# Optimization experiments

Measured on AMD Instinct MI355X. Metric: run time of the kernel, lower is better.

## Reference

```python
import jax, jax.numpy as jnp
import numpy as np

# Static geometry constants (match input_specs / init_kwargs)
B, NP, C_IN = 16, 4096, 64          # clouds, points per cloud, feature dim
RATIO, RAD = 0.25, 0.2
M = int(RATIO * NP)
HID, OUT = 64, 128


def setup_inputs() -> dict:
    key = jax.random.key(0)
    ks = jax.random.split(key, 8)
    point = jax.random.uniform(ks[0], (B * NP, 3), dtype=jnp.float32)
    xyz = jax.random.normal(ks[1], (B * NP, C_IN), dtype=jnp.float32)
    batch = jnp.arange(B * NP, dtype=jnp.int32) // NP  # contiguous equal-size clouds
    s = 0.05
    W1 = jax.random.normal(ks[2], (C_IN + 3, HID), dtype=jnp.float32) * s
    b1 = jnp.zeros((HID,), jnp.float32)
    W2 = jax.random.normal(ks[3], (HID, HID), dtype=jnp.float32) * s
    b2 = jnp.zeros((HID,), jnp.float32)
    W3 = jax.random.normal(ks[4], (HID, OUT), dtype=jnp.float32) * s
    b3 = jnp.zeros((OUT,), jnp.float32)
    return {"xyz": xyz, "point": point, "batch": batch, "num_samples": 64,
            "W1": W1, "b1": b1, "W2": W2, "b2": b2, "W3": W3, "b3": b3}


def _fps(p):
    """Farthest point sampling on one cloud p:[NP,3] -> [M] local indices (start at 0)."""
    d0 = jnp.sum((p - p[0]) ** 2, axis=-1)
    def step(d, _):
        nxt = jnp.argmax(d).astype(jnp.int32)
        d = jnp.minimum(d, jnp.sum((p - p[nxt]) ** 2, axis=-1))
        return d, nxt
    _, rest = jax.lax.scan(step, d0, None, length=M - 1)
    return jnp.concatenate([jnp.zeros((1,), jnp.int32), rest])


def reference(xyz, point, batch, num_samples, W1, b1, W2, b2, W3, b3):
    K = int(num_samples)
    pos = point.reshape(B, NP, 3)
    feat = xyz.reshape(B, NP, C_IN)

    # fps(point, batch, ratio)
    idx = jax.vmap(_fps)(pos)                                      # [B,M]
    centers = jnp.take_along_axis(pos, idx[..., None], axis=1)      # [B,M,3]

    # radius(point, point[idx], rad, max_num_neighbors=K): take K nearest in-ball
    d2 = jnp.sum((centers[:, :, None, :] - pos[:, None, :, :]) ** 2, axis=-1)  # [B,M,NP]
    valid = d2 < RAD * RAD
    sel = jnp.where(valid, d2, jnp.inf)
    _, nidx = jax.lax.top_k(-jax.lax.stop_gradient(sel), K)         # [B,M,K]
    mask = jnp.take_along_axis(valid, nidx, axis=2)                 # [B,M,K]

    # PointConv: msg = local_nn(cat([x_j, pos_j - pos_i])), aggr = max
    bi = jnp.arange(B)[:, None, None]
    pos_j = pos[bi, nidx]                                           # [B,M,K,3]
    feat_j = feat[bi, nidx]                                         # [B,M,K,C]
    msg = jnp.concatenate([feat_j, pos_j - centers[:, :, None, :]], axis=-1)
    h = jax.nn.relu(msg @ W1 + b1)
    h = jax.nn.relu(h @ W2 + b2)
    h = jax.nn.relu(h @ W3 + b3)                                    # [B,M,K,OUT]
    h = jnp.where(mask[..., None], h, -jnp.inf)
    out = jnp.max(h, axis=2).reshape(B * M, OUT)

    idx_g = (idx + jnp.arange(B, dtype=jnp.int32)[:, None] * NP).reshape(-1)
    return out, centers.reshape(B * M, 3), batch[idx_g]
```

## Files before the change

kernel.cpp:

```cpp
#include <hip/hip_runtime.h>
#include <cstdint>

#define NB 16
#define NP 4096
#define MC 1024
#define KNN 64
#define CIN 64
#define HID 64
#define OUTD 128

typedef __attribute__((ext_vector_type(8))) short bf16x8;
typedef __attribute__((ext_vector_type(4))) float f32x4;
typedef __attribute__((ext_vector_type(2))) float f32x2;
typedef unsigned long long ull;
typedef unsigned short ushort_t;

#define F32_INF __int_as_float(0x7f800000)

__device__ __forceinline__ float dist2e(float ax, float ay, float az,
                                        float bx, float by, float bz) {
  float dx = __fsub_rn(ax, bx);
  float dy = __fsub_rn(ay, by);
  float dz = __fsub_rn(az, bz);
  return __fadd_rn(__fadd_rn(__fmul_rn(dx, dx), __fmul_rn(dy, dy)), __fmul_rn(dz, dz));
}

__device__ __forceinline__ ushort_t f2bf(float f) {
  unsigned u = __float_as_uint(f);
  unsigned r = (u + 0x7FFFu + ((u >> 16) & 1u)) >> 16;
  return (ushort_t)r;
}

template <int CTRL>
__device__ __forceinline__ ull kshift(ull k) {
  int lo = (int)(unsigned)(k & 0xffffffffULL);
  int hi = (int)(unsigned)(k >> 32);
  lo = __builtin_amdgcn_update_dpp(lo, lo, CTRL, 0xf, 0xf, false);
  hi = __builtin_amdgcn_update_dpp(hi, hi, CTRL, 0xf, 0xf, false);
  return ((ull)(unsigned)hi << 32) | (ull)(unsigned)lo;
}
template <int CTRL>
__device__ __forceinline__ ull kred(ull k) {
  ull o = kshift<CTRL>(k);
  return (o > k) ? o : k;
}

__device__ __forceinline__ void wfrag_entry(const float* __restrict__ W,
                                            ushort_t* __restrict__ out,
                                            int e, int KS, int K, int N) {
  int lane = e & 63, t2 = e >> 6;
  int ks = t2 % KS, nt = t2 / KS;
  int n = nt * 16 + (lane & 15);
  int kb = ks * 32 + ((lane >> 4) & 3) * 8;
#pragma unroll
  for (int j = 0; j < 8; ++j) {
    int k = kb + j;
    float v = (k < K) ? W[(size_t)k * N + n] : 0.f;
    out[(size_t)e * 8 + j] = f2bf(v);
  }
}

__global__ __launch_bounds__(256) void fps_prep_kernel(
    const float* __restrict__ point, const float* __restrict__ xyz,
    const float* __restrict__ W1, const float* __restrict__ W2, const float* __restrict__ W3,
    float* __restrict__ ctr, float* __restrict__ cent_out, float* __restrict__ batch_out,
    ushort_t* __restrict__ xyzbf, ushort_t* __restrict__ w1f,
    ushort_t* __restrict__ w2f, ushort_t* __restrict__ w3f) {
#pragma clang fp contract(off)
  const int blk = blockIdx.x;
  const int t = threadIdx.x;
  if (blk >= NB) {
    const int pb = blk - NB;
    if (pb < 4096) {
      size_t i = ((size_t)pb * 256 + t) * 4;
      float4 v = *(const float4*)(xyz + i);
      unsigned lo = (unsigned)f2bf(v.x) | ((unsigned)f2bf(v.y) << 16);
      unsigned hi = (unsigned)f2bf(v.z) | ((unsigned)f2bf(v.w) << 16);
      uint2 o; o.x = lo; o.y = hi;
      *(uint2*)(xyzbf + i) = o;
    } else {
      for (int e = t; e < 4 * 3 * 64; e += 256) wfrag_entry(W1, w1f, e, 3, CIN + 3, HID);
      for (int e = t; e < 4 * 2 * 64; e += 256) wfrag_entry(W2, w2f, e, 2, HID, HID);
      for (int e = t; e < 8 * 2 * 64; e += 256) wfrag_entry(W3, w3f, e, 2, HID, OUTD);
    }
    return;
  }
  const int b = blk;
  const int lane = t & 63, wid = t >> 6;
  __shared__ float4 pts[NP];
  __shared__ ull kbuf[2][4];
  __shared__ int whist[MC];
  const float* p = point + (size_t)b * NP * 3;
  for (int i = t; i < NP; i += 256) {
    float4 v; v.x = p[3 * i]; v.y = p[3 * i + 1]; v.z = p[3 * i + 2]; v.w = 0.f;
    pts[i] = v;
  }
  if (t == 0) whist[0] = 0;
  __syncthreads();
  f32x2 qx2[8], qy2[8], qz2[8], d2v[8];
#pragma unroll
  for (int k = 0; k < 8; ++k) {
    float4 v0 = pts[t * 16 + 2 * k];
    float4 v1 = pts[t * 16 + 2 * k + 1];
    qx2[k].x = v0.x; qx2[k].y = v1.x;
    qy2[k].x = v0.y; qy2[k].y = v1.y;
    qz2[k].x = v0.z; qz2[k].y = v1.z;
    d2v[k].x = F32_INF; d2v[k].y = F32_INF;
  }
  int w = 0;
  for (int it = 1; it < MC; ++it) {
    float4 wp = pts[w];
    f32x2 wxx; wxx.x = wp.x; wxx.y = wp.x;
    f32x2 wyy; wyy.x = wp.y; wyy.y = wp.y;
    f32x2 wzz; wzz.x = wp.z; wzz.y = wp.z;
    float bd = -1.0f; int br = 0;
#pragma unroll
    for (int k = 0; k < 8; ++k) {
      f32x2 dx = qx2[k] - wxx;
      f32x2 dy = qy2[k] - wyy;
      f32x2 dz = qz2[k] - wzz;
      f32x2 nd = (dx * dx + dy * dy) + dz * dz;
      f32x2 dv;
      dv.x = fminf(d2v[k].x, nd.x);
      dv.y = fminf(d2v[k].y, nd.y);
      d2v[k] = dv;
      bool p1 = dv.y > dv.x;
      float pd = p1 ? dv.y : dv.x;
      int pr = 2 * k + (p1 ? 1 : 0);
      if (pd > bd) { bd = pd; br = pr; }
    }
    unsigned gi = (unsigned)(t * 16 + br);
    ull key = ((ull)__float_as_uint(bd) << 32) | (ull)(unsigned)~gi;
    key = kred<0x111>(key);
    key = kred<0x112>(key);
    key = kred<0x114>(key);
    key = kred<0x118>(key);
    key = kred<0x142>(key);
    key = kred<0x143>(key);
    const int par = it & 1;
    if (lane == 63) kbuf[par][wid] = key;
    __syncthreads();
    ull k0 = kbuf[par][0], k1 = kbuf[par][1], k2 = kbuf[par][2], k3 = kbuf[par][3];
    ull ka = (k0 > k1) ? k0 : k1;
    ull kb = (k2 > k3) ? k2 : k3;
    ull km = (ka > kb) ? ka : kb;
    w = (int)~(unsigned)(km & 0xffffffffULL);
    if (t == 0) whist[it] = w;
  }
  __syncthreads();
  for (int s = t; s < MC; s += 256) {
    int wi = whist[s];
    float4 wp = pts[wi];
    size_t o = (size_t)b * MC + s;
    ctr[3*o] = wp.x; ctr[3*o+1] = wp.y; ctr[3*o+2] = wp.z;
    cent_out[3*o] = wp.x; cent_out[3*o+1] = wp.y; cent_out[3*o+2] = wp.z;
    batch_out[o] = (float)b;
  }
}

__global__ void neigh_kernel(const float* __restrict__ point,
                             const float* __restrict__ ctr,
                             int* __restrict__ nidx, int* __restrict__ ncnt) {
  const int c = blockIdx.x;
  const int b = c >> 10;
  const int lane = threadIdx.x;
  __shared__ float ld[512];
  __shared__ int li[512];
  const float R2 = (float)(0.2 * 0.2);
  const float cx = ctr[3*c], cy = ctr[3*c+1], cz = ctr[3*c+2];
  const float* p = point + (size_t)b * NP * 3;
  int cnt = 0;
  for (int s = 0; s < NP / 64; ++s) {
    int j = s * 64 + lane;
    float d2 = dist2e(cx, cy, cz, p[3*j], p[3*j+1], p[3*j+2]);
    bool v = d2 < R2;
    ull m = __ballot(v);
    if (v) {
      int pos = cnt + __popcll(m & ((1ull << lane) - 1ull));
      if (pos < 512) { ld[pos] = d2; li[pos] = j; }
    }
    cnt += __popcll(m);
  }
  if (cnt > 512) cnt = 512;
  __syncthreads();
  if (cnt <= KNN) {
    nidx[(size_t)c * KNN + lane] = (lane < cnt) ? li[lane] : 0;
  } else {
    unsigned ob[8]; int oi[8];
#pragma unroll
    for (int r = 0; r < 8; ++r) {
      int s2 = lane + r * 64;
      if (s2 < cnt) { ob[r] = __float_as_uint(ld[s2]); oi[r] = li[s2]; }
      else { ob[r] = 0xFFFFFFFFu; oi[r] = 0; }
    }
    unsigned L = 0u, H = 0x3D23D70Au;
    while (L < H) {
      unsigned mid = (L + H) >> 1;
      int cle = 0;
#pragma unroll
      for (int r = 0; r < 8; ++r) cle += (int)__popcll(__ballot(ob[r] <= mid));
      if (cle >= KNN) H = mid; else L = mid + 1;
    }
    const unsigned tau = H;
    int c_lt = 0;
#pragma unroll
    for (int r = 0; r < 8; ++r) c_lt += (int)__popcll(__ballot(ob[r] < tau));
    const int need = KNN - c_lt;
    const ull below = (1ull << lane) - 1ull;
    int outpos = 0, eqc = 0;
#pragma unroll
    for (int r = 0; r < 8; ++r) {
      ull meq = __ballot(ob[r] == tau);
      int eqrank = eqc + (int)__popcll(meq & below);
      bool sel = (ob[r] < tau) || ((ob[r] == tau) && (eqrank < need));
      ull msel = __ballot(sel);
      if (sel) {
        int posn = outpos + (int)__popcll(msel & below);
        nidx[(size_t)c * KNN + posn] = oi[r];
      }
      outpos += (int)__popcll(msel);
      eqc += (int)__popcll(meq);
    }
  }
  if (lane == 0) ncnt[c] = (cnt < KNN) ? cnt : KNN;
}

#define HSTRIDE 72
__global__ __launch_bounds__(256) void mlp_kernel(
    const ushort_t* __restrict__ xyzbf, const float* __restrict__ point,
    const float* __restrict__ ctr, const int* __restrict__ nidx,
    const int* __restrict__ ncnt,
    const ushort_t* __restrict__ w1f, const ushort_t* __restrict__ w2f,
    const ushort_t* __restrict__ w3f,
    const float* __restrict__ b1, const float* __restrict__ b2,
    const float* __restrict__ b3,
    float* __restrict__ out) {
  const int wv = threadIdx.x >> 6, lane = threadIdx.x & 63;
  const int quad = lane >> 4, col16 = lane & 15;
  const int c = blockIdx.x * 4 + wv;
  const int bcl = c >> 10;
  const size_t bbase = (size_t)bcl * NP;
  __shared__ ushort_t hbuf_all[4 * 64 * HSTRIDE];
  ushort_t* hb = hbuf_all + wv * 64 * HSTRIDE;

  const int jg = nidx[(size_t)c * KNN + lane];
  const int nv = ncnt[c];
  const float cx = ctr[3*c], cy = ctr[3*c+1], cz = ctr[3*c+2];
  const float* pp = point + (bbase + jg) * 3;
  const float dx = pp[0] - cx, dy = pp[1] - cy, dz = pp[2] - cz;

  bf16x8 a1[4][2];
  bf16x8 a2[4];
#pragma unroll
  for (int mt = 0; mt < 4; ++mt) {
    int srcl = mt * 16 + col16;
    int jmt = __shfl(jg, srcl);
    const ushort_t* rp = xyzbf + (bbase + (size_t)jmt) * CIN + quad * 8;
    a1[mt][0] = *(const bf16x8*)(rp);
    a1[mt][1] = *(const bf16x8*)(rp + 32);
    float ddx = __shfl(dx, srcl), ddy = __shfl(dy, srcl), ddz = __shfl(dz, srcl);
    bf16x8 t2 = {0, 0, 0, 0, 0, 0, 0, 0};
    if (quad == 0) {
      t2[0] = (short)f2bf(ddx); t2[1] = (short)f2bf(ddy); t2[2] = (short)f2bf(ddz);
    }
    a2[mt] = t2;
  }

  bf16x8 bw1[4][3];
#pragma unroll
  for (int nt = 0; nt < 4; ++nt)
#pragma unroll
    for (int ks = 0; ks < 3; ++ks)
      bw1[nt][ks] = *(const bf16x8*)(w1f + ((size_t)(nt * 3 + ks) * 64 + lane) * 8);
  f32x4 acc1[4][4];
#pragma unroll
  for (int nt = 0; nt < 4; ++nt) {
    float bv = b1[nt * 16 + col16];
#pragma unroll
    for (int mt = 0; mt < 4; ++mt) { f32x4 v = {bv, bv, bv, bv}; acc1[mt][nt] = v; }
  }
#pragma unroll
  for (int mt = 0; mt < 4; ++mt)
#pragma unroll
    for (int nt = 0; nt < 4; ++nt) {
      acc1[mt][nt] = __builtin_amdgcn_mfma_f32_16x16x32_bf16(a1[mt][0], bw1[nt][0], acc1[mt][nt], 0, 0, 0);
      acc1[mt][nt] = __builtin_amdgcn_mfma_f32_16x16x32_bf16(a1[mt][1], bw1[nt][1], acc1[mt][nt], 0, 0, 0);
      acc1[mt][nt] = __builtin_amdgcn_mfma_f32_16x16x32_bf16(a2[mt],    bw1[nt][2], acc1[mt][nt], 0, 0, 0);
    }
#pragma unroll
  for (int mt = 0; mt < 4; ++mt)
#pragma unroll
    for (int nt = 0; nt < 4; ++nt)
#pragma unroll
      for (int reg = 0; reg < 4; ++reg) {
        int row = quad * 4 + reg + mt * 16;
        hb[row * HSTRIDE + col16 + nt * 16] = f2bf(fmaxf(acc1[mt][nt][reg], 0.f));
      }

  bf16x8 a21[4][2];
#pragma unroll
  for (int mt = 0; mt < 4; ++mt)
#pragma unroll
    for (int ks = 0; ks < 2; ++ks)
      a21[mt][ks] = *(const bf16x8*)(hb + (col16 + mt * 16) * HSTRIDE + ks * 32 + quad * 8);
  bf16x8 bw2[4][2];
#pragma unroll
  for (int nt = 0; nt < 4; ++nt)
#pragma unroll
    for (int ks = 0; ks < 2; ++ks)
      bw2[nt][ks] = *(const bf16x8*)(w2f + ((size_t)(nt * 2 + ks) * 64 + lane) * 8);
  f32x4 acc2[4][4];
#pragma unroll
  for (int nt = 0; nt < 4; ++nt) {
    float bv = b2[nt * 16 + col16];
#pragma unroll
    for (int mt = 0; mt < 4; ++mt) { f32x4 v = {bv, bv, bv, bv}; acc2[mt][nt] = v; }
  }
#pragma unroll
  for (int mt = 0; mt < 4; ++mt)
#pragma unroll
    for (int nt = 0; nt < 4; ++nt) {
      acc2[mt][nt] = __builtin_amdgcn_mfma_f32_16x16x32_bf16(a21[mt][0], bw2[nt][0], acc2[mt][nt], 0, 0, 0);
      acc2[mt][nt] = __builtin_amdgcn_mfma_f32_16x16x32_bf16(a21[mt][1], bw2[nt][1], acc2[mt][nt], 0, 0, 0);
    }
#pragma unroll
  for (int mt = 0; mt < 4; ++mt)
#pragma unroll
    for (int nt = 0; nt < 4; ++nt)
#pragma unroll
      for (int reg = 0; reg < 4; ++reg) {
        int row = quad * 4 + reg + mt * 16;
        hb[row * HSTRIDE + col16 + nt * 16] = f2bf(fmaxf(acc2[mt][nt][reg], 0.f));
      }

  bf16x8 a3[4][2];
#pragma unroll
  for (int mt = 0; mt < 4; ++mt)
#pragma unroll
    for (int ks = 0; ks < 2; ++ks)
      a3[mt][ks] = *(const bf16x8*)(hb + (col16 + mt * 16) * HSTRIDE + ks * 32 + quad * 8);
#pragma unroll
  for (int pass = 0; pass < 2; ++pass) {
    bf16x8 bw3[4][2];
#pragma unroll
    for (int nt = 0; nt < 4; ++nt)
#pragma unroll
      for (int ks = 0; ks < 2; ++ks)
        bw3[nt][ks] = *(const bf16x8*)(w3f + ((size_t)((pass * 4 + nt) * 2 + ks) * 64 + lane) * 8);
    f32x4 acc3[4][4];
#pragma unroll
    for (int nt = 0; nt < 4; ++nt) {
      float bv = b3[pass * 64 + nt * 16 + col16];
#pragma unroll
      for (int mt = 0; mt < 4; ++mt) { f32x4 v = {bv, bv, bv, bv}; acc3[mt][nt] = v; }
    }
#pragma unroll
    for (int mt = 0; mt < 4; ++mt)
#pragma unroll
      for (int nt = 0; nt < 4; ++nt) {
        acc3[mt][nt] = __builtin_amdgcn_mfma_f32_16x16x32_bf16(a3[mt][0], bw3[nt][0], acc3[mt][nt], 0, 0, 0);
        acc3[mt][nt] = __builtin_amdgcn_mfma_f32_16x16x32_bf16(a3[mt][1], bw3[nt][1], acc3[mt][nt], 0, 0, 0);
      }
#pragma unroll
    for (int nt = 0; nt < 4; ++nt) {
      float m = -1.0e30f;
#pragma unroll
      for (int mt = 0; mt < 4; ++mt)
#pragma unroll
        for (int reg = 0; reg < 4; ++reg) {
          int row = quad * 4 + reg + mt * 16;
          float v = fmaxf(acc3[mt][nt][reg], 0.f);
          m = fmaxf(m, (row < nv) ? v : -1.0e30f);
        }
      m = fmaxf(m, __shfl_xor(m, 16));
      m = fmaxf(m, __shfl_xor(m, 32));
      if (quad == 0)
        out[(size_t)c * OUTD + pass * 64 + nt * 16 + col16] = m;
    }
  }
}

extern "C" void kernel_launch(void* const* d_in, const int* in_sizes, int n_in,
                              void* d_out, int out_size, void* d_ws, size_t ws_size,
                              hipStream_t stream) {
  const float* xyz   = (const float*)d_in[0];
  const float* point = (const float*)d_in[1];
  const float* W1 = (const float*)d_in[4];
  const float* b1 = (const float*)d_in[5];
  const float* W2 = (const float*)d_in[6];
  const float* b2 = (const float*)d_in[7];
  const float* W3 = (const float*)d_in[8];
  const float* b3 = (const float*)d_in[9];

  float* out       = (float*)d_out;
  float* cent_out  = out + (size_t)NB * MC * OUTD;
  float* batch_out = cent_out + (size_t)NB * MC * 3;

  char* ws = (char*)d_ws;
  float* ctr       = (float*)(ws);
  int*   nidx      = (int*)(ws + 196608);
  int*   ncnt      = (int*)(ws + 196608 + 4194304);
  ushort_t* xyzbf  = (ushort_t*)(ws + 4456448);
  ushort_t* w1f    = (ushort_t*)(ws + 4456448 + 8388608);
  ushort_t* w2f    = (ushort_t*)(ws + 12845056 + 12288);
  ushort_t* w3f    = (ushort_t*)(ws + 12857344 + 8192);

  fps_prep_kernel<<<NB + 4096 + 1, 256, 0, stream>>>(
      point, xyz, W1, W2, W3, ctr, cent_out, batch_out, xyzbf, w1f, w2f, w3f);
  neigh_kernel<<<NB * MC, 64, 0, stream>>>(point, ctr, nidx, ncnt);
  mlp_kernel<<<NB * MC / 4, 256, 0, stream>>>(xyzbf, point, ctr, nidx, ncnt,
                                              w1f, w2f, w3f, b1, b2, b3, out);
}
```

Measured before the change: 850.1 us.

## Fuse FPS, neighbor search and MLP into persistent kernel with streamed center flags

Replaces the three-kernel pipeline with one persistent kernel. Sixteen blocks run farthest point sampling and publish each chosen index to global memory as soon as it is picked. The remaining 240 blocks poll those flags, then do the ball query and the MLP per center in the same wave, keeping weight fragments in LDS. This overlaps the long serial FPS with the neighbor/MLP work and drops the nidx/ctr and bf16 xyz workspace round-trips, at the cost of spin-waiting, on-the-fly bf16 conversion of features, and a reliance on FPS blocks being co-resident with the consumer blocks (256 blocks total) so the polling cannot deadlock.

```diff
diff --git a/kernel.cpp b/kernel.cpp
--- a/kernel.cpp
+++ b/kernel.cpp
@@ -16,6 +16,7 @@
 typedef unsigned short ushort_t;
 
 #define F32_INF __int_as_float(0x7f800000)
+#define WSENT 0xFFFFFFFFu
 
 __device__ __forceinline__ float dist2e(float ax, float ay, float az,
                                         float bx, float by, float bz) {
@@ -60,322 +61,341 @@
   }
 }
 
-__global__ __launch_bounds__(256) void fps_prep_kernel(
+__global__ void init_widx(unsigned* __restrict__ widx) {
+  int i = blockIdx.x * 256 + threadIdx.x;
+  if (i < NB * MC) widx[i] = WSENT;
+}
+
+__global__ __launch_bounds__(256) void mega_kernel(
     const float* __restrict__ point, const float* __restrict__ xyz,
     const float* __restrict__ W1, const float* __restrict__ W2, const float* __restrict__ W3,
-    float* __restrict__ ctr, float* __restrict__ cent_out, float* __restrict__ batch_out,
-    ushort_t* __restrict__ xyzbf, ushort_t* __restrict__ w1f,
-    ushort_t* __restrict__ w2f, ushort_t* __restrict__ w3f) {
+    const float* __restrict__ b1, const float* __restrict__ b2, const float* __restrict__ b3,
+    unsigned* __restrict__ widx,
+    float* __restrict__ out, float* __restrict__ cent_out, float* __restrict__ batch_out) {
 #pragma clang fp contract(off)
+  __shared__ char __attribute__((aligned(16))) smem[74752];
   const int blk = blockIdx.x;
   const int t = threadIdx.x;
-  if (blk >= NB) {
-    const int pb = blk - NB;
-    if (pb < 4096) {
-      size_t i = ((size_t)pb * 256 + t) * 4;
-      float4 v = *(const float4*)(xyz + i);
-      unsigned lo = (unsigned)f2bf(v.x) | ((unsigned)f2bf(v.y) << 16);
-      unsigned hi = (unsigned)f2bf(v.z) | ((unsigned)f2bf(v.w) << 16);
-      uint2 o; o.x = lo; o.y = hi;
-      *(uint2*)(xyzbf + i) = o;
-    } else {
-      for (int e = t; e < 4 * 3 * 64; e += 256) wfrag_entry(W1, w1f, e, 3, CIN + 3, HID);
-      for (int e = t; e < 4 * 2 * 64; e += 256) wfrag_entry(W2, w2f, e, 2, HID, HID);
-      for (int e = t; e < 8 * 2 * 64; e += 256) wfrag_entry(W3, w3f, e, 2, HID, OUTD);
+
+  if (blk < NB) {
+    const int b = blk;
+    const int lane = t & 63, wid = t >> 6;
+    float4* pts = (float4*)smem;
+    ull* kbuf = (ull*)(smem + 65536);
+    int* whist = (int*)(smem + 65600);
+    const float* p = point + (size_t)b * NP * 3;
+    for (int i = t; i < NP; i += 256) {
+      float4 v; v.x = p[3 * i]; v.y = p[3 * i + 1]; v.z = p[3 * i + 2]; v.w = 0.f;
+      pts[i] = v;
+    }
+    if (t == 0) {
+      whist[0] = 0;
+      __hip_atomic_store(widx + (size_t)b * MC, 0u, __ATOMIC_RELAXED, __HIP_MEMORY_SCOPE_AGENT);
+    }
+    __syncthreads();
+    f32x2 qx2[8], qy2[8], qz2[8], d2v[8];
+#pragma unroll
+    for (int k = 0; k < 8; ++k) {
+      float4 v0 = pts[t * 16 + 2 * k];
+      float4 v1 = pts[t * 16 + 2 * k + 1];
+      qx2[k].x = v0.x; qx2[k].y = v1.x;
+      qy2[k].x = v0.y; qy2[k].y = v1.y;
+      qz2[k].x = v0.z; qz2[k].y = v1.z;
+      d2v[k].x = F32_INF; d2v[k].y = F32_INF;
+    }
+    int w = 0;
+    for (int it = 1; it < MC; ++it) {
+      float4 wp = pts[w];
+      f32x2 wxx; wxx.x = wp.x; wxx.y = wp.x;
+      f32x2 wyy; wyy.x = wp.y; wyy.y = wp.y;
+      f32x2 wzz; wzz.x = wp.z; wzz.y = wp.z;
+      float bd = -1.0f; int br = 0;
+#pragma unroll
+      for (int k = 0; k < 8; ++k) {
+        f32x2 dx = qx2[k] - wxx;
+        f32x2 dy = qy2[k] - wyy;
+        f32x2 dz = qz2[k] - wzz;
+        f32x2 nd = (dx * dx + dy * dy) + dz * dz;
+        f32x2 dv;
+        dv.x = fminf(d2v[k].x, nd.x);
+        dv.y = fminf(d2v[k].y, nd.y);
+        d2v[k] = dv;
+        bool p1 = dv.y > dv.x;
+        float pd = p1 ? dv.y : dv.x;
+        int pr = 2 * k + (p1 ? 1 : 0);
+        if (pd > bd) { bd = pd; br = pr; }
+      }
+      unsigned gi = (unsigned)(t * 16 + br);
+      ull key = ((ull)__float_as_uint(bd) << 32) | (ull)(unsigned)~gi;
+      key = kred<0x111>(key);
+      key = kred<0x112>(key);
+      key = kred<0x114>(key);
+      key = kred<0x118>(key);
+      key = kred<0x142>(key);
+      key = kred<0x143>(key);
+      const int par = it & 1;
+      if (lane == 63) kbuf[par * 4 + wid] = key;
+      __syncthreads();
+      ull k0 = kbuf[par * 4 + 0], k1 = kbuf[par * 4 + 1];
+      ull k2 = kbuf[par * 4 + 2], k3 = kbuf[par * 4 + 3];
+      ull ka = (k0 > k1) ? k0 : k1;
+      ull kb = (k2 > k3) ? k2 : k3;
+      ull km = (ka > kb) ? ka : kb;
+      w = (int)~(unsigned)(km & 0xffffffffULL);
+      if (t == 0) {
+        whist[it] = w;
+        __hip_atomic_store(widx + (size_t)b * MC + it, (unsigned)w,
+                           __ATOMIC_RELAXED, __HIP_MEMORY_SCOPE_AGENT);
+      }
+    }
+    __syncthreads();
+    for (int s = t; s < MC; s += 256) {
+      int wi = whist[s];
+      float4 wp = pts[wi];
+      size_t o = (size_t)b * MC + s;
+      cent_out[3*o] = wp.x; cent_out[3*o+1] = wp.y; cent_out[3*o+2] = wp.z;
+      batch_out[o] = (float)b;
     }
     return;
   }
-  const int b = blk;
-  const int lane = t & 63, wid = t >> 6;
-  __shared__ float4 pts[NP];
-  __shared__ ull kbuf[2][4];
-  __shared__ int whist[MC];
-  const float* p = point + (size_t)b * NP * 3;
-  for (int i = t; i < NP; i += 256) {
-    float4 v; v.x = p[3 * i]; v.y = p[3 * i + 1]; v.z = p[3 * i + 2]; v.w = 0.f;
-    pts[i] = v;
-  }
-  if (t == 0) whist[0] = 0;
+
+  const int wv = t >> 6, lane = t & 63;
+  const int quad = lane >> 4, col16 = lane & 15;
+  ushort_t* w1L = (ushort_t*)smem;
+  ushort_t* w2L = (ushort_t*)(smem + 12288);
+  ushort_t* w3L = (ushort_t*)(smem + 20480);
+  for (int e = t; e < 4 * 3 * 64; e += 256) wfrag_entry(W1, w1L, e, 3, CIN + 3, HID);
+  for (int e = t; e < 4 * 2 * 64; e += 256) wfrag_entry(W2, w2L, e, 2, HID, HID);
+  for (int e = t; e < 8 * 2 * 64; e += 256) wfrag_entry(W3, w3L, e, 2, HID, OUTD);
   __syncthreads();
-  f32x2 qx2[8], qy2[8], qz2[8], d2v[8];
-#pragma unroll
-  for (int k = 0; k < 8; ++k) {
-    float4 v0 = pts[t * 16 + 2 * k];
-    float4 v1 = pts[t * 16 + 2 * k + 1];
-    qx2[k].x = v0.x; qx2[k].y = v1.x;
-    qy2[k].x = v0.y; qy2[k].y = v1.y;
-    qz2[k].x = v0.z; qz2[k].y = v1.z;
-    d2v[k].x = F32_INF; d2v[k].y = F32_INF;
-  }
-  int w = 0;
-  for (int it = 1; it < MC; ++it) {
-    float4 wp = pts[w];
-    f32x2 wxx; wxx.x = wp.x; wxx.y = wp.x;
-    f32x2 wyy; wyy.x = wp.y; wyy.y = wp.y;
-    f32x2 wzz; wzz.x = wp.z; wzz.y = wp.z;
-    float bd = -1.0f; int br = 0;
-#pragma unroll
-    for (int k = 0; k < 8; ++k) {
-      f32x2 dx = qx2[k] - wxx;
-      f32x2 dy = qy2[k] - wyy;
-      f32x2 dz = qz2[k] - wzz;
-      f32x2 nd = (dx * dx + dy * dy) + dz * dz;
-      f32x2 dv;
-      dv.x = fminf(d2v[k].x, nd.x);
-      dv.y = fminf(d2v[k].y, nd.y);
-      d2v[k] = dv;
-      bool p1 = dv.y > dv.x;
-      float pd = p1 ? dv.y : dv.x;
-      int pr = 2 * k + (p1 ? 1 : 0);
-      if (pd > bd) { bd = pd; br = pr; }
-    }
-    unsigned gi = (unsigned)(t * 16 + br);
-    ull key = ((ull)__float_as_uint(bd) << 32) | (ull)(unsigned)~gi;
-    key = kred<0x111>(key);
-    key = kred<0x112>(key);
-    key = kred<0x114>(key);
-    key = kred<0x118>(key);
-    key = kred<0x142>(key);
-    key = kred<0x143>(key);
-    const int par = it & 1;
-    if (lane == 63) kbuf[par][wid] = key;
-    __syncthreads();
-    ull k0 = kbuf[par][0], k1 = kbuf[par][1], k2 = kbuf[par][2], k3 = kbuf[par][3];
-    ull ka = (k0 > k1) ? k0 : k1;
-    ull kb = (k2 > k3) ? k2 : k3;
-    ull km = (ka > kb) ? ka : kb;
-    w = (int)~(unsigned)(km & 0xffffffffULL);
-    if (t == 0) whist[it] = w;
-  }
-  __syncthreads();
-  for (int s = t; s < MC; s += 256) {
-    int wi = whist[s];
-    float4 wp = pts[wi];
-    size_t o = (size_t)b * MC + s;
-    ctr[3*o] = wp.x; ctr[3*o+1] = wp.y; ctr[3*o+2] = wp.z;
-    cent_out[3*o] = wp.x; cent_out[3*o+1] = wp.y; cent_out[3*o+2] = wp.z;
-    batch_out[o] = (float)b;
-  }
-}
-
-__global__ void neigh_kernel(const float* __restrict__ point,
-                             const float* __restrict__ ctr,
-                             int* __restrict__ nidx, int* __restrict__ ncnt) {
-  const int c = blockIdx.x;
-  const int b = c >> 10;
-  const int lane = threadIdx.x;
-  __shared__ float ld[512];
-  __shared__ int li[512];
+
+  char* base = smem + 36864 + wv * 9472;
+  float* ld = (float*)base;
+  int* li = (int*)(base + 2048);
+  ushort_t* hb = (ushort_t*)base;
+  int* nsel = (int*)(base + 9216);
   const float R2 = (float)(0.2 * 0.2);
-  const float cx = ctr[3*c], cy = ctr[3*c+1], cz = ctr[3*c+2];
-  const float* p = point + (size_t)b * NP * 3;
-  int cnt = 0;
-  for (int s = 0; s < NP / 64; ++s) {
-    int j = s * 64 + lane;
-    float d2 = dist2e(cx, cy, cz, p[3*j], p[3*j+1], p[3*j+2]);
-    bool v = d2 < R2;
-    ull m = __ballot(v);
-    if (v) {
-      int pos = cnt + __popcll(m & ((1ull << lane) - 1ull));
-      if (pos < 512) { ld[pos] = d2; li[pos] = j; }
-    }
-    cnt += __popcll(m);
-  }
-  if (cnt > 512) cnt = 512;
-  __syncthreads();
-  if (cnt <= KNN) {
-    nidx[(size_t)c * KNN + lane] = (lane < cnt) ? li[lane] : 0;
-  } else {
-    unsigned ob[8]; int oi[8];
-#pragma unroll
-    for (int r = 0; r < 8; ++r) {
-      int s2 = lane + r * 64;
-      if (s2 < cnt) { ob[r] = __float_as_uint(ld[s2]); oi[r] = li[s2]; }
-      else { ob[r] = 0xFFFFFFFFu; oi[r] = 0; }
-    }
-    unsigned L = 0u, H = 0x3D23D70Au;
-    while (L < H) {
-      unsigned mid = (L + H) >> 1;
-      int cle = 0;
-#pragma unroll
-      for (int r = 0; r < 8; ++r) cle += (int)__popcll(__ballot(ob[r] <= mid));
-      if (cle >= KNN) H = mid; else L = mid + 1;
-    }
-    const unsigned tau = H;
-    int c_lt = 0;
-#pragma unroll
-    for (int r = 0; r < 8; ++r) c_lt += (int)__popcll(__ballot(ob[r] < tau));
-    const int need = KNN - c_lt;
-    const ull below = (1ull << lane) - 1ull;
-    int outpos = 0, eqc = 0;
-#pragma unroll
-    for (int r = 0; r < 8; ++r) {
-      ull meq = __ballot(ob[r] == tau);
-      int eqrank = eqc + (int)__popcll(meq & below);
-      bool sel = (ob[r] < tau) || ((ob[r] == tau) && (eqrank < need));
-      ull msel = __ballot(sel);
-      if (sel) {
-        int posn = outpos + (int)__popcll(msel & below);
-        nidx[(size_t)c * KNN + posn] = oi[r];
-      }
-      outpos += (int)__popcll(msel);
-      eqc += (int)__popcll(meq);
-    }
-  }
-  if (lane == 0) ncnt[c] = (cnt < KNN) ? cnt : KNN;
-}
-
-#define HSTRIDE 72
-__global__ __launch_bounds__(256) void mlp_kernel(
-    const ushort_t* __restrict__ xyzbf, const float* __restrict__ point,
-    const float* __restrict__ ctr, const int* __restrict__ nidx,
-    const int* __restrict__ ncnt,
-    const ushort_t* __restrict__ w1f, const ushort_t* __restrict__ w2f,
-    const ushort_t* __restrict__ w3f,
-    const float* __restrict__ b1, const float* __restrict__ b2,
-    const float* __restrict__ b3,
-    float* __restrict__ out) {
-  const int wv = threadIdx.x >> 6, lane = threadIdx.x & 63;
-  const int quad = lane >> 4, col16 = lane & 15;
-  const int c = blockIdx.x * 4 + wv;
-  const int bcl = c >> 10;
-  const size_t bbase = (size_t)bcl * NP;
-  __shared__ ushort_t hbuf_all[4 * 64 * HSTRIDE];
-  ushort_t* hb = hbuf_all + wv * 64 * HSTRIDE;
-
-  const int jg = nidx[(size_t)c * KNN + lane];
-  const int nv = ncnt[c];
-  const float cx = ctr[3*c], cy = ctr[3*c+1], cz = ctr[3*c+2];
-  const float* pp = point + (bbase + jg) * 3;
-  const float dx = pp[0] - cx, dy = pp[1] - cy, dz = pp[2] - cz;
-
-  bf16x8 a1[4][2];
-  bf16x8 a2[4];
-#pragma unroll
-  for (int mt = 0; mt < 4; ++mt) {
-    int srcl = mt * 16 + col16;
-    int jmt = __shfl(jg, srcl);
-    const ushort_t* rp = xyzbf + (bbase + (size_t)jmt) * CIN + quad * 8;
-    a1[mt][0] = *(const bf16x8*)(rp);
-    a1[mt][1] = *(const bf16x8*)(rp + 32);
-    float ddx = __shfl(dx, srcl), ddy = __shfl(dy, srcl), ddz = __shfl(dz, srcl);
-    bf16x8 t2 = {0, 0, 0, 0, 0, 0, 0, 0};
-    if (quad == 0) {
-      t2[0] = (short)f2bf(ddx); t2[1] = (short)f2bf(ddy); t2[2] = (short)f2bf(ddz);
-    }
-    a2[mt] = t2;
-  }
-
-  bf16x8 bw1[4][3];
-#pragma unroll
-  for (int nt = 0; nt < 4; ++nt)
-#pragma unroll
-    for (int ks = 0; ks < 3; ++ks)
-      bw1[nt][ks] = *(const bf16x8*)(w1f + ((size_t)(nt * 3 + ks) * 64 + lane) * 8);
-  f32x4 acc1[4][4];
-#pragma unroll
-  for (int nt = 0; nt < 4; ++nt) {
-    float bv = b1[nt * 16 + col16];
-#pragma unroll
-    for (int mt = 0; mt < 4; ++mt) { f32x4 v = {bv, bv, bv, bv}; acc1[mt][nt] = v; }
-  }
-#pragma unroll
-  for (int mt = 0; mt < 4; ++mt)
+  const int gwave = (blk - NB) * 4 + wv;
+
+  for (int r = gwave; r < NB * MC; r += 960) {
+    const int s = r >> 4, b = r & 15;
+    const int c = b * MC + s;
+    const size_t bbase = (size_t)b * NP;
+    unsigned wpub = 0;
+    if (lane == 0) {
+      wpub = __hip_atomic_load(widx + c, __ATOMIC_RELAXED, __HIP_MEMORY_SCOPE_AGENT);
+      while (wpub == WSENT) {
+        __builtin_amdgcn_s_sleep(32);
+        wpub = __hip_atomic_load(widx + c, __ATOMIC_RELAXED, __HIP_MEMORY_SCOPE_AGENT);
+      }
+    }
+    const int wc = __shfl((int)wpub, 0);
+    const float cx = point[(bbase + wc) * 3];
+    const float cy = point[(bbase + wc) * 3 + 1];
+    const float cz = point[(bbase + wc) * 3 + 2];
+
+    const float* p = point + bbase * 3;
+    int cnt = 0;
+    for (int sb = 0; sb < NP / 64; ++sb) {
+      int j = sb * 64 + lane;
+      float d2 = dist2e(cx, cy, cz, p[3*j], p[3*j+1], p[3*j+2]);
+      bool v = d2 < R2;
+      ull m = __ballot(v);
+      if (v) {
+        int pos = cnt + __popcll(m & ((1ull << lane) - 1ull));
+        if (pos < 512) { ld[pos] = d2; li[pos] = j; }
+      }
+      cnt += __popcll(m);
+    }
+    if (cnt > 512) cnt = 512;
+    asm volatile("s_waitcnt lgkmcnt(0)" ::: "memory");
+    if (cnt <= KNN) {
+      nsel[lane] = (lane < cnt) ? li[lane] : 0;
+    } else {
+      unsigned ob[8]; int oi[8];
+#pragma unroll
+      for (int rr = 0; rr < 8; ++rr) {
+        int s2 = lane + rr * 64;
+        if (s2 < cnt) { ob[rr] = __float_as_uint(ld[s2]); oi[rr] = li[s2]; }
+        else { ob[rr] = 0xFFFFFFFFu; oi[rr] = 0; }
+      }
+      unsigned L = 0u, H = 0x3D23D70Au;
+      while (L < H) {
+        unsigned mid = (L + H) >> 1;
+        int cle = 0;
+#pragma unroll
+        for (int rr = 0; rr < 8; ++rr) cle += (int)__popcll(__ballot(ob[rr] <= mid));
+        if (cle >= KNN) H = mid; else L = mid + 1;
+      }
+      const unsigned tau = H;
+      int c_lt = 0;
+#pragma unroll
+      for (int rr = 0; rr < 8; ++rr) c_lt += (int)__popcll(__ballot(ob[rr] < tau));
+      const int need = KNN - c_lt;
+      const ull below = (1ull << lane) - 1ull;
+      int outpos = 0, eqc = 0;
+#pragma unroll
+      for (int rr = 0; rr < 8; ++rr) {
+        ull meq = __ballot(ob[rr] == tau);
+        int eqrank = eqc + (int)__popcll(meq & below);
+        bool sel = (ob[rr] < tau) || ((ob[rr] == tau) && (eqrank < need));
+        ull msel = __ballot(sel);
+        if (sel) {
+          int posn = outpos + (int)__popcll(msel & below);
+          nsel[posn] = oi[rr];
+        }
+        outpos += (int)__popcll(msel);
+        eqc += (int)__popcll(meq);
+      }
+    }
+    const int nv = (cnt < KNN) ? cnt : KNN;
+    asm volatile("s_waitcnt lgkmcnt(0)" ::: "memory");
+    const int jg = nsel[lane];
+
+    const float* pp = point + (bbase + jg) * 3;
+    const float dxx = pp[0] - cx, dyy = pp[1] - cy, dzz = pp[2] - cz;
+
+    bf16x8 a1[4][2];
+    bf16x8 a2[4];
+#pragma unroll
+    for (int mt = 0; mt < 4; ++mt) {
+      int srcl = mt * 16 + col16;
+      int jmt = __shfl(jg, srcl);
+      const float* xr = xyz + (bbase + (size_t)jmt) * CIN + quad * 8;
+      float4 f0 = *(const float4*)(xr);
+      float4 f1 = *(const float4*)(xr + 4);
+      float4 f2 = *(const float4*)(xr + 32);
+      float4 f3 = *(const float4*)(xr + 36);
+      bf16x8 v0, v1;
+      v0[0] = (short)f2bf(f0.x); v0[1] = (short)f2bf(f0.y);
+      v0[2] = (short)f2bf(f0.z); v0[3] = (short)f2bf(f0.w);
+      v0[4] = (short)f2bf(f1.x); v0[5] = (short)f2bf(f1.y);
+      v0[6] = (short)f2bf(f1.z); v0[7] = (short)f2bf(f1.w);
+      v1[0] = (short)f2bf(f2.x); v1[1] = (short)f2bf(f2.y);
+      v1[2] = (short)f2bf(f2.z); v1[3] = (short)f2bf(f2.w);
+      v1[4] = (short)f2bf(f3.x); v1[5] = (short)f2bf(f3.y);
+      v1[6] = (short)f2bf(f3.z); v1[7] = (short)f2bf(f3.w);
+      a1[mt][0] = v0;
+      a1[mt][1] = v1;
+      float ddx = __shfl(dxx, srcl), ddy = __shfl(dyy, srcl), ddz = __shfl(dzz, srcl);
+      bf16x8 t2 = {0, 0, 0, 0, 0, 0, 0, 0};
+      if (quad == 0) {
+        t2[0] = (short)f2bf(ddx); t2[1] = (short)f2bf(ddy); t2[2] = (short)f2bf(ddz);
+      }
+      a2[mt] = t2;
+    }
+
+    bf16x8 bw1[4][3];
+#pragma unroll
+    for (int nt = 0; nt < 4; ++nt)
+#pragma unroll
+      for (int ks = 0; ks < 3; ++ks)
+        bw1[nt][ks] = *(const bf16x8*)(w1L + ((size_t)(nt * 3 + ks) * 64 + lane) * 8);
+    f32x4 acc1[4][4];
 #pragma unroll
     for (int nt = 0; nt < 4; ++nt) {
-      acc1[mt][nt] = __builtin_amdgcn_mfma_f32_16x16x32_bf16(a1[mt][0], bw1[nt][0], acc1[mt][nt], 0, 0, 0);
-      acc1[mt][nt] = __builtin_amdgcn_mfma_f32_16x16x32_bf16(a1[mt][1], bw1[nt][1], acc1[mt][nt], 0, 0, 0);
-      acc1[mt][nt] = __builtin_amdgcn_mfma_f32_16x16x32_bf16(a2[mt],    bw1[nt][2], acc1[mt][nt], 0, 0, 0);
-    }
-#pragma unroll
-  for (int mt = 0; mt < 4; ++mt)
-#pragma unroll
-    for (int nt = 0; nt < 4; ++nt)
-#pragma unroll
-      for (int reg = 0; reg < 4; ++reg) {
-        int row = quad * 4 + reg + mt * 16;
-        hb[row * HSTRIDE + col16 + nt * 16] = f2bf(fmaxf(acc1[mt][nt][reg], 0.f));
-      }
-
-  bf16x8 a21[4][2];
-#pragma unroll
-  for (int mt = 0; mt < 4; ++mt)
-#pragma unroll
-    for (int ks = 0; ks < 2; ++ks)
-      a21[mt][ks] = *(const bf16x8*)(hb + (col16 + mt * 16) * HSTRIDE + ks * 32 + quad * 8);
-  bf16x8 bw2[4][2];
-#pragma unroll
-  for (int nt = 0; nt < 4; ++nt)
-#pragma unroll
-    for (int ks = 0; ks < 2; ++ks)
-      bw2[nt][ks] = *(const bf16x8*)(w2f + ((size_t)(nt * 2 + ks) * 64 + lane) * 8);
-  f32x4 acc2[4][4];
-#pragma unroll
-  for (int nt = 0; nt < 4; ++nt) {
-    float bv = b2[nt * 16 + col16];
-#pragma unroll
-    for (int mt = 0; mt < 4; ++mt) { f32x4 v = {bv, bv, bv, bv}; acc2[mt][nt] = v; }
-  }
-#pragma unroll
-  for (int mt = 0; mt < 4; ++mt)
-#pragma unroll
-    for (int nt = 0; nt < 4; ++nt) {
-      acc2[mt][nt] = __builtin_amdgcn_mfma_f32_16x16x32_bf16(a21[mt][0], bw2[nt][0], acc2[mt][nt], 0, 0, 0);
-      acc2[mt][nt] = __builtin_amdgcn_mfma_f32_16x16x32_bf16(a21[mt][1], bw2[nt][1], acc2[mt][nt], 0, 0, 0);
-    }
-#pragma unroll
-  for (int mt = 0; mt < 4; ++mt)
-#pragma unroll
-    for (int nt = 0; nt < 4; ++nt)
-#pragma unroll
-      for (int reg = 0; reg < 4; ++reg) {
-        int row = quad * 4 + reg + mt * 16;
-        hb[row * HSTRIDE + col16 + nt * 16] = f2bf(fmaxf(acc2[mt][nt][reg], 0.f));
-      }
-
-  bf16x8 a3[4][2];
-#pragma unroll
-  for (int mt = 0; mt < 4; ++mt)
-#pragma unroll
-    for (int ks = 0; ks < 2; ++ks)
-      a3[mt][ks] = *(const bf16x8*)(hb + (col16 + mt * 16) * HSTRIDE + ks * 32 + quad * 8);
-#pragma unroll
-  for (int pass = 0; pass < 2; ++pass) {
-    bf16x8 bw3[4][2];
-#pragma unroll
-    for (int nt = 0; nt < 4; ++nt)
-#pragma unroll
-      for (int ks = 0; ks < 2; ++ks)
-        bw3[nt][ks] = *(const bf16x8*)(w3f + ((size_t)((pass * 4 + nt) * 2 + ks) * 64 + lane) * 8);
-    f32x4 acc3[4][4];
-#pragma unroll
-    for (int nt = 0; nt < 4; ++nt) {
-      float bv = b3[pass * 64 + nt * 16 + col16];
-#pragma unroll
-      for (int mt = 0; mt < 4; ++mt) { f32x4 v = {bv, bv, bv, bv}; acc3[mt][nt] = v; }
+      float bv = b1[nt * 16 + col16];
+#pragma unroll
+      for (int mt = 0; mt < 4; ++mt) { f32x4 v = {bv, bv, bv, bv}; acc1[mt][nt] = v; }
     }
 #pragma unroll
     for (int mt = 0; mt < 4; ++mt)
 #pragma unroll
       for (int nt = 0; nt < 4; ++nt) {
-        acc3[mt][nt] = __builtin_amdgcn_mfma_f32_16x16x32_bf16(a3[mt][0], bw3[nt][0], acc3[mt][nt], 0, 0, 0);
-        acc3[mt][nt] = __builtin_amdgcn_mfma_f32_16x16x32_bf16(a3[mt][1], bw3[nt][1], acc3[mt][nt], 0, 0, 0);
-      }
-#pragma unroll
-    for (int nt = 0; nt < 4; ++nt) {
-      float m = -1.0e30f;
-#pragma unroll
-      for (int mt = 0; mt < 4; ++mt)
+        acc1[mt][nt] = __builtin_amdgcn_mfma_f32_16x16x32_bf16(a1[mt][0], bw1[nt][0], acc1[mt][nt], 0, 0, 0);
+        acc1[mt][nt] = __builtin_amdgcn_mfma_f32_16x16x32_bf16(a1[mt][1], bw1[nt][1], acc1[mt][nt], 0, 0, 0);
+        acc1[mt][nt] = __builtin_amdgcn_mfma_f32_16x16x32_bf16(a2[mt],    bw1[nt][2], acc1[mt][nt], 0, 0, 0);
+      }
+#pragma unroll
+    for (int mt = 0; mt < 4; ++mt)
+#pragma unroll
+      for (int nt = 0; nt < 4; ++nt)
 #pragma unroll
         for (int reg = 0; reg < 4; ++reg) {
           int row = quad * 4 + reg + mt * 16;
-          float v = fmaxf(acc3[mt][nt][reg], 0.f);
-          m = fmaxf(m, (row < nv) ? v : -1.0e30f);
+          hb[row * 72 + col16 + nt * 16] = f2bf(fmaxf(acc1[mt][nt][reg], 0.f));
         }
-      m = fmaxf(m, __shfl_xor(m, 16));
-      m = fmaxf(m, __shfl_xor(m, 32));
-      if (quad == 0)
-        out[(size_t)c * OUTD + pass * 64 + nt * 16 + col16] = m;
+
+    bf16x8 a21[4][2];
+#pragma unroll
+    for (int mt = 0; mt < 4; ++mt)
+#pragma unroll
+      for (int ks = 0; ks < 2; ++ks)
+        a21[mt][ks] = *(const bf16x8*)(hb + (col16 + mt * 16) * 72 + ks * 32 + quad * 8);
+    bf16x8 bw2[4][2];
+#pragma unroll
+    for (int nt = 0; nt < 4; ++nt)
+#pragma unroll
+      for (int ks = 0; ks < 2; ++ks)
+        bw2[nt][ks] = *(const bf16x8*)(w2L + ((size_t)(nt * 2 + ks) * 64 + lane) * 8);
+    f32x4 acc2[4][4];
+#pragma unroll
+    for (int nt = 0; nt < 4; ++nt) {
+      float bv = b2[nt * 16 + col16];
+#pragma unroll
+      for (int mt = 0; mt < 4; ++mt) { f32x4 v = {bv, bv, bv, bv}; acc2[mt][nt] = v; }
+    }
+#pragma unroll
+    for (int mt = 0; mt < 4; ++mt)
+#pragma unroll
+      for (int nt = 0; nt < 4; ++nt) {
+        acc2[mt][nt] = __builtin_amdgcn_mfma_f32_16x16x32_bf16(a21[mt][0], bw2[nt][0], acc2[mt][nt], 0, 0, 0);
+        acc2[mt][nt] = __builtin_amdgcn_mfma_f32_16x16x32_bf16(a21[mt][1], bw2[nt][1], acc2[mt][nt], 0, 0, 0);
+      }
+#pragma unroll
+    for (int mt = 0; mt < 4; ++mt)
+#pragma unroll
+      for (int nt = 0; nt < 4; ++nt)
+#pragma unroll
+        for (int reg = 0; reg < 4; ++reg) {
+          int row = quad * 4 + reg + mt * 16;
+          hb[row * 72 + col16 + nt * 16] = f2bf(fmaxf(acc2[mt][nt][reg], 0.f));
+        }
+
+    bf16x8 a3[4][2];
+#pragma unroll
+    for (int mt = 0; mt < 4; ++mt)
+#pragma unroll
+      for (int ks = 0; ks < 2; ++ks)
+        a3[mt][ks] = *(const bf16x8*)(hb + (col16 + mt * 16) * 72 + ks * 32 + quad * 8);
+#pragma unroll
+    for (int pass = 0; pass < 2; ++pass) {
+      bf16x8 bw3[4][2];
+#pragma unroll
+      for (int nt = 0; nt < 4; ++nt)
+#pragma unroll
+        for (int ks = 0; ks < 2; ++ks)
+          bw3[nt][ks] = *(const bf16x8*)(w3L + ((size_t)((pass * 4 + nt) * 2 + ks) * 64 + lane) * 8);
+      f32x4 acc3[4][4];
+#pragma unroll
+      for (int nt = 0; nt < 4; ++nt) {
+        float bv = b3[pass * 64 + nt * 16 + col16];
+#pragma unroll
+        for (int mt = 0; mt < 4; ++mt) { f32x4 v = {bv, bv, bv, bv}; acc3[mt][nt] = v; }
+      }
+#pragma unroll
+      for (int mt = 0; mt < 4; ++mt)
+#pragma unroll
+        for (int nt = 0; nt < 4; ++nt) {
+          acc3[mt][nt] = __builtin_amdgcn_mfma_f32_16x16x32_bf16(a3[mt][0], bw3[nt][0], acc3[mt][nt], 0, 0, 0);
+          acc3[mt][nt] = __builtin_amdgcn_mfma_f32_16x16x32_bf16(a3[mt][1], bw3[nt][1], acc3[mt][nt], 0, 0, 0);
+        }
+#pragma unroll
+      for (int nt = 0; nt < 4; ++nt) {
+        float m = -1.0e30f;
+#pragma unroll
+        for (int mt = 0; mt < 4; ++mt)
+#pragma unroll
+          for (int reg = 0; reg < 4; ++reg) {
+            int row = quad * 4 + reg + mt * 16;
+            float v = fmaxf(acc3[mt][nt][reg], 0.f);
+            m = fmaxf(m, (row < nv) ? v : -1.0e30f);
+          }
+        m = fmaxf(m, __shfl_xor(m, 16));
+        m = fmaxf(m, __shfl_xor(m, 32));
+        if (quad == 0)
+          out[(size_t)c * OUTD + pass * 64 + nt * 16 + col16] = m;
+      }
     }
   }
 }
@@ -396,18 +416,9 @@
   float* cent_out  = out + (size_t)NB * MC * OUTD;
   float* batch_out = cent_out + (size_t)NB * MC * 3;
 
-  char* ws = (char*)d_ws;
-  float* ctr       = (float*)(ws);
-  int*   nidx      = (int*)(ws + 196608);
-  int*   ncnt      = (int*)(ws + 196608 + 4194304);
-  ushort_t* xyzbf  = (ushort_t*)(ws + 4456448);
-  ushort_t* w1f    = (ushort_t*)(ws + 4456448 + 8388608);
-  ushort_t* w2f    = (ushort_t*)(ws + 12845056 + 12288);
-  ushort_t* w3f    = (ushort_t*)(ws + 12857344 + 8192);
-
-  fps_prep_kernel<<<NB + 4096 + 1, 256, 0, stream>>>(
-      point, xyz, W1, W2, W3, ctr, cent_out, batch_out, xyzbf, w1f, w2f, w3f);
-  neigh_kernel<<<NB * MC, 64, 0, stream>>>(point, ctr, nidx, ncnt);
-  mlp_kernel<<<NB * MC / 4, 256, 0, stream>>>(xyzbf, point, ctr, nidx, ncnt,
-                                              w1f, w2f, w3f, b1, b2, b3, out);
-}
+  unsigned* widx = (unsigned*)d_ws;
+
+  init_widx<<<64, 256, 0, stream>>>(widx);
+  mega_kernel<<<256, 256, 0, stream>>>(point, xyz, W1, W2, W3, b1, b2, b3,
+                                       widx, out, cent_out, batch_out);
+}
```

Result: faster. 754.0 us (-11.3%).
